# Kernel optimization log

Hardware: AMD Instinct MI355X
Metric: run time of the kernel (lower is better)

Reference implementation:

```python
import jax, jax.numpy as jnp
import numpy as np

D_MODEL = 1024
D_STATE = 32
EXPAND = 2
D_INNER = D_MODEL * EXPAND
B_SZ = 2
SEQ = 512


def setup_inputs() -> dict:
    key = jax.random.key(0)
    ks = jax.random.split(key, 10)
    x = jax.random.normal(ks[0], (B_SZ, SEQ, D_MODEL), dtype=jnp.float32)
    W_in = jax.random.normal(ks[1], (2 * D_INNER, D_MODEL), dtype=jnp.float32) * 0.02
    A_log = jax.random.uniform(ks[2], (D_INNER, D_STATE), minval=-4.0, maxval=-1.0, dtype=jnp.float32)
    W_B = jax.random.normal(ks[3], (D_STATE, D_MODEL), dtype=jnp.float32) * 0.02
    W_C = jax.random.normal(ks[4], (D_STATE, D_MODEL), dtype=jnp.float32) * 0.02
    W_dt = jax.random.normal(ks[5], (D_INNER, D_MODEL), dtype=jnp.float32) * 0.02
    b_dt = jnp.zeros((D_INNER,), dtype=jnp.float32)
    dt_bias = jnp.zeros((D_INNER,), dtype=jnp.float32) - 4.0
    rope_freq = jax.random.normal(ks[6], (D_STATE // 2,), dtype=jnp.float32) * 0.01
    ln_w = jnp.ones((D_INNER,), dtype=jnp.float32)
    ln_b = jnp.zeros((D_INNER,), dtype=jnp.float32)
    W_out = jax.random.normal(ks[7], (D_MODEL, D_INNER), dtype=jnp.float32) * 0.02
    return {"x": x, "W_in": W_in, "A_log": A_log, "W_B": W_B, "W_C": W_C,
            "W_dt": W_dt, "b_dt": b_dt, "dt_bias": dt_bias, "rope_freq": rope_freq,
            "ln_w": ln_w, "ln_b": ln_b, "W_out": W_out}


def _forward(x, W_in, A_log, W_B, W_C, W_dt, b_dt, dt_bias, rope_freq, ln_w, ln_b, W_out):
    B, L, _ = x.shape
    half = D_STATE // 2
    offset = 0

    xz = jnp.einsum('bld,ed->ble', x, W_in)                 # [B,L,2*D_INNER]
    x_inner = xz[..., :D_INNER]                             # [B,L,DI]
    z = jax.nn.silu(xz[..., D_INNER:])                      # [B,L,DI]

    A = -jnp.exp(A_log)                                     # [DI,DS]
    Bm = jnp.einsum('bld,nd->bln', x, W_B)                  # [B,L,DS]
    Cm = jnp.einsum('bld,nd->bln', x, W_C)                  # [B,L,DS]
    dt = jax.nn.softplus(jnp.einsum('bld,ed->ble', x, W_dt) + b_dt + dt_bias)  # [B,L,DI]

    # trapezoidal discretization
    dtA = dt[..., None] * A                                 # [B,L,DI,DS]
    denom = 1.0 - dtA / 2.0
    A_bar = (1.0 + dtA / 2.0) / denom                       # [B,L,DI,DS]
    B_bar = dt[..., None] / denom                           # [B,L,DI,DS]

    # per-step rope rotation angles: angle_t = rope_freq * (t + offset)
    t_idx = jnp.arange(L, dtype=jnp.float32) + offset       # [L]
    ang = t_idx[:, None] * rope_freq                        # [L,half]
    cos_a = jnp.cos(ang)
    sin_a = jnp.sin(ang)

    def step(state, inp):
        A_t, Bb_t, B_t, x_t, C_t, c_t, s_t = inp
        # state update: [B,DI,DS]
        state = A_t * state + Bb_t * B_t[:, None, :] * x_t[:, :, None]
        real = state[..., :half]
        imag = state[..., half:]
        state = jnp.concatenate([real * c_t - imag * s_t,
                                 real * s_t + imag * c_t], axis=-1)
        y_t = jnp.einsum('bds,bs->bd', state, C_t)          # [B,DI]
        return state, y_t

    state0 = jnp.zeros((B, D_INNER, D_STATE), dtype=x.dtype)
    xs = (jnp.swapaxes(A_bar, 0, 1), jnp.swapaxes(B_bar, 0, 1),
          jnp.swapaxes(Bm, 0, 1), jnp.swapaxes(x_inner, 0, 1),
          jnp.swapaxes(Cm, 0, 1), cos_a, sin_a)
    final_state, ys = jax.lax.scan(step, state0, xs)        # ys: [L,B,DI]
    out = jnp.swapaxes(ys, 0, 1) * z                        # [B,L,DI]

    # LayerNorm over last dim (eps=1e-5, torch default)
    mu = jnp.mean(out, axis=-1, keepdims=True)
    var = jnp.mean((out - mu) ** 2, axis=-1, keepdims=True)
    out = (out - mu) * jax.lax.rsqrt(var + 1e-5) * ln_w + ln_b

    out = jnp.einsum('ble,de->bld', out, W_out)             # [B,L,D_MODEL]
    return out, final_state


def reference(x, W_in, A_log, W_B, W_C, W_dt, b_dt, dt_bias, rope_freq, ln_w, ln_b, W_out):
    return _forward(x, W_in, A_log, W_B, W_C, W_dt, b_dt, dt_bias, rope_freq, ln_w, ln_b, W_out)
```

## Files before the change

### kernel.cpp

```cpp
#include <hip/hip_runtime.h>
#include <math.h>

#define B_SZ 2
#define SEQ 512
#define DM 1024
#define DI 2048
#define DS 32
#define TOK (B_SZ*SEQ)
#define NCH 8
#define CLEN (SEQ/NCH)
#define NPAIRH 32768

#define NFUSED 6272

typedef float v2f __attribute__((ext_vector_type(2)));

__device__ __forceinline__ unsigned short f2bf(float f) {
  unsigned int u = __builtin_bit_cast(unsigned int, f);
  unsigned int r = u + 0x7fffu + ((u >> 16) & 1u);
  return (unsigned short)(r >> 16);
}

static __device__ __forceinline__ v2f pk_fma(v2f a, v2f b, v2f c) {
  v2f d;
  asm("v_pk_fma_f32 %0, %1, %2, %3" : "=v"(d) : "v"(a), "v"(b), "v"(c));
  return d;
}
static __device__ __forceinline__ v2f pk_fms(v2f a, v2f b, v2f c) {
  v2f d;
  asm("v_pk_fma_f32 %0, %1, %2, %3 neg_lo:[0,0,1] neg_hi:[0,0,1]"
      : "=v"(d) : "v"(a), "v"(b), "v"(c));
  return d;
}
static __device__ __forceinline__ v2f pk_mul(v2f a, v2f b) {
  v2f d;
  asm("v_pk_mul_f32 %0, %1, %2" : "=v"(d) : "v"(a), "v"(b));
  return d;
}
static __device__ __forceinline__ v2f pk_add(v2f a, v2f b) {
  v2f d;
  asm("v_pk_add_f32 %0, %1, %2" : "=v"(d) : "v"(a), "v"(b));
  return d;
}
static __device__ __forceinline__ v2f pk_fma_b(v2f a, v2f b, v2f c) {
  v2f d;
  asm("v_pk_fma_f32 %0, %1, %2, %3 op_sel_hi:[1,0,1]"
      : "=v"(d) : "v"(a), "v"(b), "v"(c));
  return d;
}
static __device__ __forceinline__ v2f pk_mul_b(v2f a, v2f b) {
  v2f d;
  asm("v_pk_mul_f32 %0, %1, %2 op_sel_hi:[1,0]"
      : "=v"(d) : "v"(a), "v"(b));
  return d;
}

template<int CTRL>
__device__ __forceinline__ float row_ror_add(float x) {
  int s = __builtin_amdgcn_update_dpp(0, __builtin_bit_cast(int, x), CTRL, 0xf, 0xf, false);
  return x + __builtin_bit_cast(float, s);
}
__device__ __forceinline__ float row16_sum(float v) {
  v = row_ror_add<0x121>(v);
  v = row_ror_add<0x122>(v);
  v = row_ror_add<0x124>(v);
  v = row_ror_add<0x128>(v);
  return v;
}

__global__ __launch_bounds__(256) void fused_cast(const float* __restrict__ x,
                                                  const float* __restrict__ W_in,
                                                  const float* __restrict__ W_dt,
                                                  const float* __restrict__ W_B,
                                                  const float* __restrict__ W_C,
                                                  const float* __restrict__ W_out,
                                                  unsigned short* __restrict__ xb,
                                                  unsigned short* __restrict__ wcat,
                                                  unsigned short* __restrict__ wob) {
  int g = blockIdx.x * 256 + threadIdx.x;
  const float* s; unsigned short* dd; int off;
  if      (g <  131072) { s = x;     dd = xb;             off = 0; }
  else if (g <  655360) { s = W_in;  dd = wcat;           off = 131072; }
  else if (g <  917504) { s = W_dt;  dd = wcat + 4194304; off = 655360; }
  else if (g <  921600) { s = W_B;   dd = wcat + 6291456; off = 917504; }
  else if (g <  925696) { s = W_C;   dd = wcat + 6324224; off = 921600; }
  else if (g < 1187840) { s = W_out; dd = wob;            off = 925696; }
  else return;
  int i = g - off;
  float4 a = ((const float4*)s)[i * 2];
  float4 b = ((const float4*)s)[i * 2 + 1];
  union { unsigned short us[8]; uint4 v; } o;
  o.us[0] = f2bf(a.x); o.us[1] = f2bf(a.y); o.us[2] = f2bf(a.z); o.us[3] = f2bf(a.w);
  o.us[4] = f2bf(b.x); o.us[5] = f2bf(b.y); o.us[6] = f2bf(b.z); o.us[7] = f2bf(b.w);
  ((uint4*)dd)[i] = o.v;
}

typedef __attribute__((ext_vector_type(8))) short  frag8;
typedef __attribute__((ext_vector_type(4))) float  facc4;

__device__ __forceinline__ void gload_lds16(const unsigned short* g, unsigned short* l) {
  __builtin_amdgcn_global_load_lds((const __attribute__((address_space(1))) unsigned int*)g,
                                   (__attribute__((address_space(3))) unsigned int*)l, 16, 0, 0);
}
__device__ __forceinline__ void gload_lds16f(const float* g, float* l) {
  __builtin_amdgcn_global_load_lds((const __attribute__((address_space(1))) unsigned int*)g,
                                   (__attribute__((address_space(3))) unsigned int*)l, 16, 0, 0);
}

__device__ __forceinline__ float softplus_fast(float v) {
  return fmaxf(v, 0.f) + __logf(1.f + __expf(-fabsf(v)));
}

__global__ __launch_bounds__(256) void gemm1_big(const unsigned short* __restrict__ A,
                                                 const unsigned short* __restrict__ Bw,
                                                 float* __restrict__ o_xs,
                                                 float* __restrict__ o_zb,
                                                 float* __restrict__ o_dts,
                                                 float* __restrict__ o_bcb,
                                                 const float* __restrict__ b_dt,
                                                 const float* __restrict__ dt_bias) {
  __shared__ __align__(16) unsigned short As[128 * 64];
  __shared__ __align__(16) unsigned short Bs[64 * 64];
  const int K = DM;
  const int tid = threadIdx.x;
  const int w = tid >> 6, lane = tid & 63;
  const int wm = w >> 1, wn = w & 1;
  const int bid = blockIdx.x;
  const int Wk = (bid & 7) * 98 + (bid >> 3);
  const int m0 = (Wk & 7) * 128;
  const int n0 = (Wk >> 3) * 64;
  const int r = lane & 15, q = lane >> 4;
  const int srow = lane >> 3;
  const int scol = ((lane & 7) ^ srow) * 8;
  facc4 acc[4][2] = {};
  const unsigned short* Ag = A + (size_t)m0 * K;
  const unsigned short* Bg = Bw + (size_t)n0 * K;

  for (int k0 = 0; k0 < DM; k0 += 64) {
#pragma unroll
    for (int k = 0; k < 4; ++k) {
      int ch = w * 4 + k;
      gload_lds16(Ag + (size_t)(ch * 8 + srow) * K + k0 + scol, &As[ch * 512]);
    }
#pragma unroll
    for (int k = 0; k < 2; ++k) {
      int ch = w * 2 + k;
      gload_lds16(Bg + (size_t)(ch * 8 + srow) * K + k0 + scol, &Bs[ch * 512]);
    }
    __syncthreads();
#pragma unroll
    for (int kk = 0; kk < 2; ++kk) {
      frag8 af[4], bfr[2];
      const int sw = ((kk * 4 + q) ^ (r & 7)) * 8;
#pragma unroll
      for (int i = 0; i < 4; ++i)
        af[i] = *(const frag8*)&As[(wm * 64 + i * 16 + r) * 64 + sw];
#pragma unroll
      for (int jj = 0; jj < 2; ++jj)
        bfr[jj] = *(const frag8*)&Bs[(wn * 32 + jj * 16 + r) * 64 + sw];
#pragma unroll
      for (int i = 0; i < 4; ++i)
#pragma unroll
        for (int jj = 0; jj < 2; ++jj)
          acc[i][jj] = __builtin_amdgcn_mfma_f32_16x16x32_bf16(af[i], bfr[jj], acc[i][jj], 0, 0, 0);
    }
    __syncthreads();
  }

#pragma unroll
  for (int i = 0; i < 4; ++i) {
#pragma unroll
    for (int jj = 0; jj < 2; ++jj) {
      int n = n0 + wn * 32 + jj * 16 + r;
      int mb = m0 + wm * 64 + i * 16 + q * 4;
      if (n < 2048) {
#pragma unroll
        for (int rg = 0; rg < 4; ++rg)
          o_xs[(size_t)(mb + rg) * DI + n] = acc[i][jj][rg];
      } else if (n < 4096) {
#pragma unroll
        for (int rg = 0; rg < 4; ++rg)
          o_zb[(size_t)(mb + rg) * DI + (n - 2048)] = acc[i][jj][rg];
      } else if (n < 6144) {
        int d = n - 4096;
        float bias = b_dt[d] + dt_bias[d];
#pragma unroll
        for (int rg = 0; rg < 4; ++rg)
          o_dts[(size_t)(mb + rg) * DI + d] = softplus_fast(acc[i][jj][rg] + bias);
      } else if (n < 6176) {
#pragma unroll
        for (int rg = 0; rg < 4; ++rg)
          o_bcb[(size_t)(mb + rg) * DS + (n - 6144)] = acc[i][jj][rg];
      } else if (n < 6208) {
#pragma unroll
        for (int rg = 0; rg < 4; ++rg)
          o_bcb[(size_t)TOK * DS + (size_t)(mb + rg) * DS + (n - 6176)] = acc[i][jj][rg];
      }
    }
  }
}

template<int MT, int NT, int KSP>
__global__ __launch_bounds__(256) void gemm_mfma(const unsigned short* __restrict__ A,
                                                 const unsigned short* __restrict__ Bw,
                                                 int K,
                                                 float* __restrict__ o_c, int ldc) {
  __shared__ __align__(16) unsigned short As[64 * 64];
  __shared__ __align__(16) unsigned short Bs[64 * 64];
  const int tid = threadIdx.x;
  const int w = tid >> 6, lane = tid & 63;
  const int wm = w >> 1, wn = w & 1;
  const int bid = blockIdx.x;
  const int Wk = (bid & 7) * ((int)gridDim.x >> 3) + (bid >> 3);
  const int ks = Wk / (MT * NT);
  const int rem = Wk % (MT * NT);
  const int m0 = (rem % MT) * 64;
  const int n0 = (rem / MT) * 64;
  const int kLen = K / KSP, kBeg = ks * kLen;
  const int r = lane & 15, q = lane >> 4;
  const int srow = lane >> 3;
  const int scol = ((lane & 7) ^ (srow & 7)) * 8;
  facc4 acc[2][2] = {};
  const unsigned short* Ag = A + (size_t)m0 * K + kBeg;
  const unsigned short* Bg = Bw + (size_t)n0 * K + kBeg;

  for (int k0 = 0; k0 < kLen; k0 += 64) {
#pragma unroll
    for (int k = 0; k < 2; ++k) {
      int ch = w * 2 + k;
      gload_lds16(Ag + (size_t)(ch * 8 + srow) * K + k0 + scol, &As[ch * 512]);
      gload_lds16(Bg + (size_t)(ch * 8 + srow) * K + k0 + scol, &Bs[ch * 512]);
    }
    __syncthreads();
#pragma unroll
    for (int kk = 0; kk < 2; ++kk) {
      frag8 af[2], bf[2];
      const int sw = ((kk * 4 + q) ^ (r & 7)) * 8;
#pragma unroll
      for (int i = 0; i < 2; ++i)
        af[i] = *(const frag8*)&As[(wm * 32 + i * 16 + r) * 64 + sw];
#pragma unroll
      for (int jj = 0; jj < 2; ++jj)
        bf[jj] = *(const frag8*)&Bs[(wn * 32 + jj * 16 + r) * 64 + sw];
#pragma unroll
      for (int i = 0; i < 2; ++i)
#pragma unroll
        for (int jj = 0; jj < 2; ++jj)
          acc[i][jj] = __builtin_amdgcn_mfma_f32_16x16x32_bf16(af[i], bf[jj], acc[i][jj], 0, 0, 0);
    }
    __syncthreads();
  }

#pragma unroll
  for (int i = 0; i < 2; ++i) {
#pragma unroll
    for (int jj = 0; jj < 2; ++jj) {
      int n = n0 + wn * 32 + jj * 16 + r;
      int mb = m0 + wm * 32 + i * 16 + q * 4;
      float* oc = o_c + (size_t)ks * (MT * 64) * ldc;
#pragma unroll
      for (int rg = 0; rg < 4; ++rg)
        oc[(size_t)(mb + rg) * ldc + n] = acc[i][jj][rg];
    }
  }
}

__global__ __launch_bounds__(256) void addk(const float* __restrict__ p0,
                                            const float* __restrict__ p1,
                                            float* __restrict__ o) {
  int i = blockIdx.x * 256 + threadIdx.x;
  float4 a = ((const float4*)p0)[i];
  float4 b = ((const float4*)p1)[i];
  ((float4*)o)[i] = make_float4(a.x + b.x, a.y + b.y, a.z + b.z, a.w + b.w);
}

__global__ __launch_bounds__(256) void scan_p1(const float* __restrict__ xs,
                                               const float* __restrict__ dts,
                                               const float* __restrict__ bcb,
                                               const float* __restrict__ A_log,
                                               const float* __restrict__ rope,
                                               float* __restrict__ Pbuf) {
  __shared__ __align__(16) float lds[6144];
  const int blk = blockIdx.x;
  const int c = blk >> 7;
  const int sub = blk & 127;
  const int b = sub >> 6;
  const int dbase = (sub & 63) << 5;
  const int tid = threadIdx.x;
  const int wv = tid >> 6, lane = tid & 63;
  const int j = tid & 15;
  const int ca = (tid >> 4) & 15;
  const int l0 = c * CLEN;
  const size_t base = (size_t)(b * SEQ + l0);

  {
    int row = wv * 16 + (lane >> 3);
    int col = (lane & 7) << 2;
#pragma unroll
    for (int k = 0; k < 2; ++k) {
      gload_lds16f(xs  + (base + row + k * 8) * DI + dbase + col, &lds[(wv * 16 + k * 8) * 32]);
      gload_lds16f(dts + (base + row + k * 8) * DI + dbase + col, &lds[2048 + (wv * 16 + k * 8) * 32]);
    }
#pragma unroll
    for (int k = 0; k < 2; ++k) {
      int seg = wv * 2 + k;
      gload_lds16f(bcb + base * DS + seg * 256 + lane * 4, &lds[4096 + seg * 256]);
    }
  }

  const int dA = dbase + 2 * ca;
  v2f Ar, Ai;
  Ar.x = -0.5f * __expf(A_log[dA * DS + j]);
  Ar.y = -0.5f * __expf(A_log[(dA + 1) * DS + j]);
  Ai.x = -0.5f * __expf(A_log[dA * DS + j + 16]);
  Ai.y = -0.5f * __expf(A_log[(dA + 1) * DS + j + 16]);
  const float fr = rope[j];
  float sn0, cs0, sFs, cFs;
  __sincosf((float)l0 * fr, &sn0, &cs0);
  __sincosf(fr, &sFs, &cFs);
  const v2f one = {1.f, 1.f};
  const v2f two = {2.f, 2.f};
  v2f cs2 = {cs0, cs0}, sn2 = {sn0, sn0};
  const v2f cF2 = {cFs, cFs}, sF2 = {sFs, sFs};
  __syncthreads();

  v2f p00 = one, p01 = {0.f, 0.f}, p10 = {0.f, 0.f}, p11 = one;
  v2f ur = {0.f, 0.f}, ui = {0.f, 0.f};

#pragma unroll 4
  for (int tt = 0; tt < CLEN; ++tt) {
    const int ro = tt * 32;
    v2f xin = *(const v2f*)&lds[ro + 2 * ca];
    v2f dtd = *(const v2f*)&lds[2048 + ro + 2 * ca];
    v2f Br2, Bi2;
    Br2.x = lds[4096 + ro + j];
    Bi2.x = lds[4096 + ro + j + 16];
    v2f hr = pk_mul(dtd, Ar), hi = pk_mul(dtd, Ai);
    v2f invr = pk_fma(hr, pk_fma(hr, pk_add(hr, one), one), one);
    v2f invi = pk_fma(hi, pk_fma(hi, pk_add(hi, one), one), one);
    v2f dx = pk_mul(dtd, xin);
    v2f gr = pk_fma_b(dx, Br2, pk_add(ur, ur));
    v2f gi = pk_fma_b(dx, Bi2, pk_add(ui, ui));
    v2f tr = pk_fms(invr, gr, ur);
    v2f ti = pk_fms(invi, gi, ui);
    ur = pk_fms(tr, cs2, pk_mul(ti, sn2));
    ui = pk_fma(tr, sn2, pk_mul(ti, cs2));
    v2f Abr = pk_fms(invr, two, one);
    v2f Abi = pk_fms(invi, two, one);
    v2f q00 = pk_mul(Abr, p00), q01 = pk_mul(Abr, p01);
    v2f q10 = pk_mul(Abi, p10), q11 = pk_mul(Abi, p11);
    p00 = pk_fms(q00, cs2, pk_mul(q10, sn2));
    p10 = pk_fma(q00, sn2, pk_mul(q10, cs2));
    p01 = pk_fms(q01, cs2, pk_mul(q11, sn2));
    p11 = pk_fma(q01, sn2, pk_mul(q11, cs2));
    v2f ocs = cs2;
    cs2 = pk_fms(cs2, cF2, pk_mul(sn2, sF2));
    sn2 = pk_fma(sn2, cF2, pk_mul(ocs, sF2));
  }
  const int pc = (b * 1024 + (dbase >> 1) + ca) * 16 + j;
  float2* Pb2 = (float2*)Pbuf;
  Pb2[(c * 6 + 0) * NPAIRH + pc] = make_float2(p00.x, p00.y);
  Pb2[(c * 6 + 1) * NPAIRH + pc] = make_float2(p01.x, p01.y);
  Pb2[(c * 6 + 2) * NPAIRH + pc] = make_float2(p10.x, p10.y);
  Pb2[(c * 6 + 3) * NPAIRH + pc] = make_float2(p11.x, p11.y);
  Pb2[(c * 6 + 4) * NPAIRH + pc] = make_float2(ur.x, ur.y);
  Pb2[(c * 6 + 5) * NPAIRH + pc] = make_float2(ui.x, ui.y);
}

__global__ __launch_bounds__(256) void scan_p3(const float* __restrict__ xs,
                                               const float* __restrict__ dts,
                                               const float* __restrict__ bcb,
                                               const float* __restrict__ A_log,
                                               const float* __restrict__ rope,
                                               const float* __restrict__ Pbuf,
                                               float* __restrict__ y,
                                               float* __restrict__ fstate) {
  __shared__ __align__(16) float lds[8192];
  const int blk = blockIdx.x;
  const int c = blk >> 7;
  const int sub = blk & 127;
  const int b = sub >> 6;
  const int dbase = (sub & 63) << 5;
  const int tid = threadIdx.x;
  const int wv = tid >> 6, lane = tid & 63;
  const int j = tid & 15;
  const int ca = (tid >> 4) & 15;
  const int l0 = c * CLEN;
  const size_t base = (size_t)(b * SEQ + l0);

  {
    int row = wv * 16 + (lane >> 3);
    int col = (lane & 7) << 2;
#pragma unroll
    for (int k = 0; k < 2; ++k) {
      gload_lds16f(xs  + (base + row + k * 8) * DI + dbase + col, &lds[(wv * 16 + k * 8) * 32]);
      gload_lds16f(dts + (base + row + k * 8) * DI + dbase + col, &lds[2048 + (wv * 16 + k * 8) * 32]);
    }
#pragma unroll
    for (int k = 0; k < 2; ++k) {
      int seg = wv * 2 + k;
      gload_lds16f(bcb + base * DS + seg * 256 + lane * 4, &lds[4096 + seg * 256]);
      gload_lds16f(bcb + (size_t)TOK * DS + base * DS + seg * 256 + lane * 4, &lds[6144 + seg * 256]);
    }
  }

  const int dA = dbase + 2 * ca;
  v2f Ar, Ai;
  Ar.x = -0.5f * __expf(A_log[dA * DS + j]);
  Ar.y = -0.5f * __expf(A_log[(dA + 1) * DS + j]);
  Ai.x = -0.5f * __expf(A_log[dA * DS + j + 16]);
  Ai.y = -0.5f * __expf(A_log[(dA + 1) * DS + j + 16]);
  const float fr = rope[j];
  float sn0, cs0, sFs, cFs;
  __sincosf((float)l0 * fr, &sn0, &cs0);
  __sincosf(fr, &sFs, &cFs);
  const v2f one = {1.f, 1.f};
  v2f cs2 = {cs0, cs0}, sn2 = {sn0, sn0};
  const v2f cF2 = {cFs, cFs}, sF2 = {sFs, sFs};

  const int pc = (b * 1024 + (dbase >> 1) + ca) * 16 + j;
  const float2* Pb2 = (const float2*)Pbuf;
  v2f sr = {0.f, 0.f}, si = {0.f, 0.f};
  for (int k = 0; k < c; ++k) {
    float2 f;
    f = Pb2[(k * 6 + 0) * NPAIRH + pc]; v2f p00 = {f.x, f.y};
    f = Pb2[(k * 6 + 1) * NPAIRH + pc]; v2f p01 = {f.x, f.y};
    f = Pb2[(k * 6 + 2) * NPAIRH + pc]; v2f p10 = {f.x, f.y};
    f = Pb2[(k * 6 + 3) * NPAIRH + pc]; v2f p11 = {f.x, f.y};
    f = Pb2[(k * 6 + 4) * NPAIRH + pc]; v2f ur  = {f.x, f.y};
    f = Pb2[(k * 6 + 5) * NPAIRH + pc]; v2f ui  = {f.x, f.y};
    v2f nr = p00 * sr + p01 * si + ur;
    v2f ni = p10 * sr + p11 * si + ui;
    sr = nr; si = ni;
  }
  __syncthreads();

  float* yp = y + base * DI + dA;

#pragma unroll 4
  for (int tt = 0; tt < CLEN; ++tt) {
    const int ro = tt * 32;
    v2f xin = *(const v2f*)&lds[ro + 2 * ca];
    v2f dtd = *(const v2f*)&lds[2048 + ro + 2 * ca];
    v2f Br2, Bi2, Cr2, Ci2;
    Br2.x = lds[4096 + ro + j];
    Bi2.x = lds[4096 + ro + j + 16];
    Cr2.x = lds[6144 + ro + j];
    Ci2.x = lds[6144 + ro + j + 16];
    v2f hr = pk_mul(dtd, Ar), hi = pk_mul(dtd, Ai);
    v2f invr = pk_fma(hr, pk_fma(hr, pk_add(hr, one), one), one);
    v2f invi = pk_fma(hi, pk_fma(hi, pk_add(hi, one), one), one);
    v2f dx = pk_mul(dtd, xin);
    v2f gr = pk_fma_b(dx, Br2, pk_add(sr, sr));
    v2f gi = pk_fma_b(dx, Bi2, pk_add(si, si));
    v2f tr = pk_fms(invr, gr, sr);
    v2f ti = pk_fms(invi, gi, si);
    sr = pk_fms(tr, cs2, pk_mul(ti, sn2));
    si = pk_fma(tr, sn2, pk_mul(ti, cs2));
    v2f p = pk_fma_b(si, Ci2, pk_mul_b(sr, Cr2));
    float pA = row16_sum(p.x);
    float pB = row16_sum(p.y);
    if (j == 0) *(float2*)&yp[tt * DI] = make_float2(pA, pB);
    v2f ocs = cs2;
    cs2 = pk_fms(cs2, cF2, pk_mul(sn2, sF2));
    sn2 = pk_fma(sn2, cF2, pk_mul(ocs, sF2));
  }
  if (c == NCH - 1) {
    fstate[((size_t)b * DI + dA) * DS + j]          = sr.x;
    fstate[((size_t)b * DI + dA) * DS + j + 16]     = si.x;
    fstate[((size_t)b * DI + dA + 1) * DS + j]      = sr.y;
    fstate[((size_t)b * DI + dA + 1) * DS + j + 16] = si.y;
  }
}

__global__ __launch_bounds__(256) void gate_ln(const float* __restrict__ y,
                                               const float* __restrict__ zb,
                                               const float* __restrict__ lw,
                                               const float* __restrict__ lb,
                                               unsigned short* __restrict__ o) {
  int tok = blockIdx.x;
  int t = threadIdx.x;
  float g[8];
  float sum = 0.f, sq = 0.f;
#pragma unroll
  for (int i = 0; i < 8; ++i) {
    int dd = t + i * 256;
    float yv = y[(size_t)tok * DI + dd];
    float zv = zb[(size_t)tok * DI + dd];
    float sg = zv / (1.f + __expf(-zv));
    float v = yv * sg;
    g[i] = v; sum += v; sq += v * v;
  }
#pragma unroll
  for (int off = 32; off; off >>= 1) { sum += __shfl_xor(sum, off); sq += __shfl_xor(sq, off); }
  __shared__ float rs[4], rq[4];
  int w = t >> 6;
  if ((t & 63) == 0) { rs[w] = sum; rq[w] = sq; }
  __syncthreads();
  sum = rs[0] + rs[1] + rs[2] + rs[3];
  sq  = rq[0] + rq[1] + rq[2] + rq[3];
  float mu = sum * (1.f / DI);
  float var = sq * (1.f / DI) - mu * mu;
  float rstd = rsqrtf(var + 1e-5f);
#pragma unroll
  for (int i = 0; i < 8; ++i) {
    int dd = t + i * 256;
    o[(size_t)tok * DI + dd] = f2bf((g[i] - mu) * rstd * lw[dd] + lb[dd]);
  }
}

extern "C" void kernel_launch(void* const* d_in, const int* in_sizes, int n_in,
                              void* d_out, int out_size, void* d_ws, size_t ws_size,
                              hipStream_t stream) {
  const float* x       = (const float*)d_in[0];
  const float* W_in    = (const float*)d_in[1];
  const float* A_log   = (const float*)d_in[2];
  const float* W_B     = (const float*)d_in[3];
  const float* W_C     = (const float*)d_in[4];
  const float* W_dt    = (const float*)d_in[5];
  const float* b_dt    = (const float*)d_in[6];
  const float* dt_bias = (const float*)d_in[7];
  const float* rope    = (const float*)d_in[8];
  const float* ln_w    = (const float*)d_in[9];
  const float* ln_b    = (const float*)d_in[10];
  const float* W_out   = (const float*)d_in[11];
  float* out = (float*)d_out;
  float* ws = (float*)d_ws;

  float* xs   = ws;
  float* zb   = ws + 2097152;
  float* dts  = ws + 4194304;
  float* bcb  = ws + 6291456;
  unsigned short* wob  = (unsigned short*)(ws + 6356992);
  unsigned short* xb   = (unsigned short*)(ws + 7405568);
  unsigned short* wcat = (unsigned short*)(ws + 7929856);
  float* Pbuf = ws + 7929856;
  float* yb   = ws + 11141120;
  unsigned short* lnb = (unsigned short*)(ws + 13238272);
  float* Pk   = ws;
  float* fstate = out + (size_t)TOK * DM;

  fused_cast<<<4640, 256, 0, stream>>>(x, W_in, W_dt, W_B, W_C, W_out, xb, wcat, wob);
  gemm1_big<<<784, 256, 0, stream>>>(xb, wcat, xs, zb, dts, bcb, b_dt, dt_bias);
  scan_p1<<<(NCH - 1) * 128, 256, 0, stream>>>(xs, dts, bcb, A_log, rope, Pbuf);
  scan_p3<<<NCH * 128, 256, 0, stream>>>(xs, dts, bcb, A_log, rope, Pbuf, yb, fstate);
  gate_ln<<<TOK, 256, 0, stream>>>(yb, zb, ln_w, ln_b, lnb);
  gemm_mfma<16, 16, 2><<<16 * 16 * 2, 256, 0, stream>>>(lnb, wob, DI, Pk, DM);
  addk<<<(TOK * DM) / 1024, 256, 0, stream>>>(Pk, Pk + (size_t)TOK * DM, out);
}
```

Baseline: 197.4 us.

## Interleave x and dt channels and B/C real-imag pairs for vector LDS reads

The GEMM epilogue now writes x_inner and dt into one interleaved buffer (x pair, dt pair per channel pair), and stores B/C with real and imaginary halves interleaved. The scan kernels load this with fewer, wider global-to-LDS copies and read x/dt as one 128-bit LDS load and B/C as one 64-bit load, using op_sel packed FMAs to select halves. This is meant to cut LDS read instructions in the serial scan loop. In exchange the GEMM epilogue stores become strided (stride 4 floats), which may hurt its write coalescing.

```diff
diff --git a/kernel.cpp b/kernel.cpp
--- a/kernel.cpp
+++ b/kernel.cpp
@@ -14,6 +14,7 @@
 #define NFUSED 6272
 
 typedef float v2f __attribute__((ext_vector_type(2)));
+typedef float v4f __attribute__((ext_vector_type(4)));
 
 __device__ __forceinline__ unsigned short f2bf(float f) {
   unsigned int u = __builtin_bit_cast(unsigned int, f);
@@ -45,6 +46,12 @@
 static __device__ __forceinline__ v2f pk_fma_b(v2f a, v2f b, v2f c) {
   v2f d;
   asm("v_pk_fma_f32 %0, %1, %2, %3 op_sel_hi:[1,0,1]"
+      : "=v"(d) : "v"(a), "v"(b), "v"(c));
+  return d;
+}
+static __device__ __forceinline__ v2f pk_fma_bh(v2f a, v2f b, v2f c) {
+  v2f d;
+  asm("v_pk_fma_f32 %0, %1, %2, %3 op_sel:[0,1,0] op_sel_hi:[1,1,1]"
       : "=v"(d) : "v"(a), "v"(b), "v"(c));
   return d;
 }
@@ -113,9 +120,8 @@
 
 __global__ __launch_bounds__(256) void gemm1_big(const unsigned short* __restrict__ A,
                                                  const unsigned short* __restrict__ Bw,
-                                                 float* __restrict__ o_xs,
+                                                 float* __restrict__ o_xdt,
                                                  float* __restrict__ o_zb,
-                                                 float* __restrict__ o_dts,
                                                  float* __restrict__ o_bcb,
                                                  const float* __restrict__ b_dt,
                                                  const float* __restrict__ dt_bias) {
@@ -176,7 +182,7 @@
       if (n < 2048) {
 #pragma unroll
         for (int rg = 0; rg < 4; ++rg)
-          o_xs[(size_t)(mb + rg) * DI + n] = acc[i][jj][rg];
+          o_xdt[(size_t)(mb + rg) * 4096 + (n >> 1) * 4 + (n & 1)] = acc[i][jj][rg];
       } else if (n < 4096) {
 #pragma unroll
         for (int rg = 0; rg < 4; ++rg)
@@ -186,15 +192,19 @@
         float bias = b_dt[d] + dt_bias[d];
 #pragma unroll
         for (int rg = 0; rg < 4; ++rg)
-          o_dts[(size_t)(mb + rg) * DI + d] = softplus_fast(acc[i][jj][rg] + bias);
+          o_xdt[(size_t)(mb + rg) * 4096 + (d >> 1) * 4 + 2 + (d & 1)] =
+              softplus_fast(acc[i][jj][rg] + bias);
       } else if (n < 6176) {
+        int d = n - 6144;
 #pragma unroll
         for (int rg = 0; rg < 4; ++rg)
-          o_bcb[(size_t)(mb + rg) * DS + (n - 6144)] = acc[i][jj][rg];
+          o_bcb[(size_t)(mb + rg) * DS + (d & 15) * 2 + (d >> 4)] = acc[i][jj][rg];
       } else if (n < 6208) {
+        int d = n - 6176;
 #pragma unroll
         for (int rg = 0; rg < 4; ++rg)
-          o_bcb[(size_t)TOK * DS + (size_t)(mb + rg) * DS + (n - 6176)] = acc[i][jj][rg];
+          o_bcb[(size_t)TOK * DS + (size_t)(mb + rg) * DS + (d & 15) * 2 + (d >> 4)] =
+              acc[i][jj][rg];
       }
     }
   }
@@ -274,8 +284,7 @@
   ((float4*)o)[i] = make_float4(a.x + b.x, a.y + b.y, a.z + b.z, a.w + b.w);
 }
 
-__global__ __launch_bounds__(256) void scan_p1(const float* __restrict__ xs,
-                                               const float* __restrict__ dts,
+__global__ __launch_bounds__(256) void scan_p1(const float* __restrict__ xdt,
                                                const float* __restrict__ bcb,
                                                const float* __restrict__ A_log,
                                                const float* __restrict__ rope,
@@ -294,13 +303,12 @@
   const size_t base = (size_t)(b * SEQ + l0);
 
   {
-    int row = wv * 16 + (lane >> 3);
-    int col = (lane & 7) << 2;
-#pragma unroll
-    for (int k = 0; k < 2; ++k) {
-      gload_lds16f(xs  + (base + row + k * 8) * DI + dbase + col, &lds[(wv * 16 + k * 8) * 32]);
-      gload_lds16f(dts + (base + row + k * 8) * DI + dbase + col, &lds[2048 + (wv * 16 + k * 8) * 32]);
-    }
+    int t = wv * 4 + (lane >> 4);
+    int col = (lane & 15) * 4;
+#pragma unroll
+    for (int k = 0; k < 4; ++k)
+      gload_lds16f(xdt + (base + k * 16 + t) * 4096 + dbase * 2 + col,
+                   &lds[(k * 16 + wv * 4) * 64]);
 #pragma unroll
     for (int k = 0; k < 2; ++k) {
       int seg = wv * 2 + k;
@@ -329,18 +337,16 @@
 
 #pragma unroll 4
   for (int tt = 0; tt < CLEN; ++tt) {
-    const int ro = tt * 32;
-    v2f xin = *(const v2f*)&lds[ro + 2 * ca];
-    v2f dtd = *(const v2f*)&lds[2048 + ro + 2 * ca];
-    v2f Br2, Bi2;
-    Br2.x = lds[4096 + ro + j];
-    Bi2.x = lds[4096 + ro + j + 16];
-    v2f hr = pk_mul(dtd, Ar), hi = pk_mul(dtd, Ai);
+    v4f xd = *(const v4f*)&lds[tt * 64 + ca * 4];
+    v2f Bv = *(const v2f*)&lds[4096 + tt * 32 + 2 * j];
+    v2f xin = {xd.x, xd.y};
+    v2f dtd = {xd.z, xd.w};
+    v2f hr = pk_mul(dtd, Ar), hi2 = pk_mul(dtd, Ai);
     v2f invr = pk_fma(hr, pk_fma(hr, pk_add(hr, one), one), one);
-    v2f invi = pk_fma(hi, pk_fma(hi, pk_add(hi, one), one), one);
+    v2f invi = pk_fma(hi2, pk_fma(hi2, pk_add(hi2, one), one), one);
     v2f dx = pk_mul(dtd, xin);
-    v2f gr = pk_fma_b(dx, Br2, pk_add(ur, ur));
-    v2f gi = pk_fma_b(dx, Bi2, pk_add(ui, ui));
+    v2f gr = pk_fma_b (dx, Bv, pk_add(ur, ur));
+    v2f gi = pk_fma_bh(dx, Bv, pk_add(ui, ui));
     v2f tr = pk_fms(invr, gr, ur);
     v2f ti = pk_fms(invi, gi, ui);
     ur = pk_fms(tr, cs2, pk_mul(ti, sn2));
@@ -367,8 +373,7 @@
   Pb2[(c * 6 + 5) * NPAIRH + pc] = make_float2(ui.x, ui.y);
 }
 
-__global__ __launch_bounds__(256) void scan_p3(const float* __restrict__ xs,
-                                               const float* __restrict__ dts,
+__global__ __launch_bounds__(256) void scan_p3(const float* __restrict__ xdt,
                                                const float* __restrict__ bcb,
                                                const float* __restrict__ A_log,
                                                const float* __restrict__ rope,
@@ -389,18 +394,18 @@
   const size_t base = (size_t)(b * SEQ + l0);
 
   {
-    int row = wv * 16 + (lane >> 3);
-    int col = (lane & 7) << 2;
-#pragma unroll
-    for (int k = 0; k < 2; ++k) {
-      gload_lds16f(xs  + (base + row + k * 8) * DI + dbase + col, &lds[(wv * 16 + k * 8) * 32]);
-      gload_lds16f(dts + (base + row + k * 8) * DI + dbase + col, &lds[2048 + (wv * 16 + k * 8) * 32]);
-    }
+    int t = wv * 4 + (lane >> 4);
+    int col = (lane & 15) * 4;
+#pragma unroll
+    for (int k = 0; k < 4; ++k)
+      gload_lds16f(xdt + (base + k * 16 + t) * 4096 + dbase * 2 + col,
+                   &lds[(k * 16 + wv * 4) * 64]);
 #pragma unroll
     for (int k = 0; k < 2; ++k) {
       int seg = wv * 2 + k;
       gload_lds16f(bcb + base * DS + seg * 256 + lane * 4, &lds[4096 + seg * 256]);
-      gload_lds16f(bcb + (size_t)TOK * DS + base * DS + seg * 256 + lane * 4, &lds[6144 + seg * 256]);
+      gload_lds16f(bcb + (size_t)TOK * DS + base * DS + seg * 256 + lane * 4,
+                   &lds[6144 + seg * 256]);
     }
   }
 
@@ -439,25 +444,22 @@
 
 #pragma unroll 4
   for (int tt = 0; tt < CLEN; ++tt) {
-    const int ro = tt * 32;
-    v2f xin = *(const v2f*)&lds[ro + 2 * ca];
-    v2f dtd = *(const v2f*)&lds[2048 + ro + 2 * ca];
-    v2f Br2, Bi2, Cr2, Ci2;
-    Br2.x = lds[4096 + ro + j];
-    Bi2.x = lds[4096 + ro + j + 16];
-    Cr2.x = lds[6144 + ro + j];
-    Ci2.x = lds[6144 + ro + j + 16];
-    v2f hr = pk_mul(dtd, Ar), hi = pk_mul(dtd, Ai);
+    v4f xd = *(const v4f*)&lds[tt * 64 + ca * 4];
+    v2f Bv = *(const v2f*)&lds[4096 + tt * 32 + 2 * j];
+    v2f Cv = *(const v2f*)&lds[6144 + tt * 32 + 2 * j];
+    v2f xin = {xd.x, xd.y};
+    v2f dtd = {xd.z, xd.w};
+    v2f hr = pk_mul(dtd, Ar), hi2 = pk_mul(dtd, Ai);
     v2f invr = pk_fma(hr, pk_fma(hr, pk_add(hr, one), one), one);
-    v2f invi = pk_fma(hi, pk_fma(hi, pk_add(hi, one), one), one);
+    v2f invi = pk_fma(hi2, pk_fma(hi2, pk_add(hi2, one), one), one);
     v2f dx = pk_mul(dtd, xin);
-    v2f gr = pk_fma_b(dx, Br2, pk_add(sr, sr));
-    v2f gi = pk_fma_b(dx, Bi2, pk_add(si, si));
+    v2f gr = pk_fma_b (dx, Bv, pk_add(sr, sr));
+    v2f gi = pk_fma_bh(dx, Bv, pk_add(si, si));
     v2f tr = pk_fms(invr, gr, sr);
     v2f ti = pk_fms(invi, gi, si);
     sr = pk_fms(tr, cs2, pk_mul(ti, sn2));
     si = pk_fma(tr, sn2, pk_mul(ti, cs2));
-    v2f p = pk_fma_b(si, Ci2, pk_mul_b(sr, Cr2));
+    v2f p = pk_fma_bh(si, Cv, pk_mul_b(sr, Cv));
     float pA = row16_sum(p.x);
     float pB = row16_sum(p.y);
     if (j == 0) *(float2*)&yp[tt * DI] = make_float2(pA, pB);
@@ -527,9 +529,8 @@
   float* out = (float*)d_out;
   float* ws = (float*)d_ws;
 
-  float* xs   = ws;
-  float* zb   = ws + 2097152;
-  float* dts  = ws + 4194304;
+  float* xdt  = ws;
+  float* zb   = ws + 4194304;
   float* bcb  = ws + 6291456;
   unsigned short* wob  = (unsigned short*)(ws + 6356992);
   unsigned short* xb   = (unsigned short*)(ws + 7405568);
@@ -541,9 +542,9 @@
   float* fstate = out + (size_t)TOK * DM;
 
   fused_cast<<<4640, 256, 0, stream>>>(x, W_in, W_dt, W_B, W_C, W_out, xb, wcat, wob);
-  gemm1_big<<<784, 256, 0, stream>>>(xb, wcat, xs, zb, dts, bcb, b_dt, dt_bias);
-  scan_p1<<<(NCH - 1) * 128, 256, 0, stream>>>(xs, dts, bcb, A_log, rope, Pbuf);
-  scan_p3<<<NCH * 128, 256, 0, stream>>>(xs, dts, bcb, A_log, rope, Pbuf, yb, fstate);
+  gemm1_big<<<784, 256, 0, stream>>>(xb, wcat, xdt, zb, bcb, b_dt, dt_bias);
+  scan_p1<<<(NCH - 1) * 128, 256, 0, stream>>>(xdt, bcb, A_log, rope, Pbuf);
+  scan_p3<<<NCH * 128, 256, 0, stream>>>(xdt, bcb, A_log, rope, Pbuf, yb, fstate);
   gate_ln<<<TOK, 256, 0, stream>>>(yb, zb, ln_w, ln_b, lnb);
   gemm_mfma<16, 16, 2><<<16 * 16 * 2, 256, 0, stream>>>(lnb, wob, DI, Pk, DM);
   addk<<<(TOK * DM) / 1024, 256, 0, stream>>>(Pk, Pk + (size_t)TOK * DM, out);
```

After: 205.6 us. +4.1%, slower.

## Double scan chunk count and fuse split-K output GEMM reduction in-block

Applied to the files above, without the earlier changes.

Raises the number of scan chunks from 8 to 16, halving chunk length so the scan kernels launch more blocks with smaller LDS tiles and shorter serial loops. The cost is a longer cross-chunk combine and a larger Pbuf, which now moves to its own workspace region. The output GEMM replaces the split-K launch plus a separate add kernel with one 512-thread block per tile. Two 256-thread groups each cover half of K and are summed through shared memory. This drops one kernel launch and the partial-sum round trip through global memory, but halves the GEMM grid to 256 blocks.

```diff
diff --git a/kernel.cpp b/kernel.cpp
--- a/kernel.cpp
+++ b/kernel.cpp
@@ -7,7 +7,7 @@
 #define DI 2048
 #define DS 32
 #define TOK (B_SZ*SEQ)
-#define NCH 8
+#define NCH 16
 #define CLEN (SEQ/NCH)
 #define NPAIRH 32768
 
@@ -200,36 +200,36 @@
   }
 }
 
-template<int MT, int NT, int KSP>
-__global__ __launch_bounds__(256) void gemm_mfma(const unsigned short* __restrict__ A,
-                                                 const unsigned short* __restrict__ Bw,
-                                                 int K,
-                                                 float* __restrict__ o_c, int ldc) {
-  __shared__ __align__(16) unsigned short As[64 * 64];
-  __shared__ __align__(16) unsigned short Bs[64 * 64];
+__global__ __launch_bounds__(512) void gemm2_fused(const unsigned short* __restrict__ A,
+                                                   const unsigned short* __restrict__ Bw,
+                                                   float* __restrict__ o_c) {
+  __shared__ __align__(16) unsigned short As[2][64 * 64];
+  __shared__ __align__(16) unsigned short Bs[2][64 * 64];
+  const int K = DI;
   const int tid = threadIdx.x;
-  const int w = tid >> 6, lane = tid & 63;
+  const int grp = tid >> 8;
+  const int w = (tid >> 6) & 3;
+  const int lane = tid & 63;
   const int wm = w >> 1, wn = w & 1;
   const int bid = blockIdx.x;
-  const int Wk = (bid & 7) * ((int)gridDim.x >> 3) + (bid >> 3);
-  const int ks = Wk / (MT * NT);
-  const int rem = Wk % (MT * NT);
-  const int m0 = (rem % MT) * 64;
-  const int n0 = (rem / MT) * 64;
-  const int kLen = K / KSP, kBeg = ks * kLen;
+  const int Wk = (bid & 7) * 32 + (bid >> 3);
+  const int m0 = (Wk % 16) * 64;
+  const int n0 = (Wk / 16) * 64;
   const int r = lane & 15, q = lane >> 4;
   const int srow = lane >> 3;
-  const int scol = ((lane & 7) ^ (srow & 7)) * 8;
+  const int scol = ((lane & 7) ^ srow) * 8;
   facc4 acc[2][2] = {};
-  const unsigned short* Ag = A + (size_t)m0 * K + kBeg;
-  const unsigned short* Bg = Bw + (size_t)n0 * K + kBeg;
-
-  for (int k0 = 0; k0 < kLen; k0 += 64) {
+  const unsigned short* Ag = A + (size_t)m0 * K + grp * 1024;
+  const unsigned short* Bg = Bw + (size_t)n0 * K + grp * 1024;
+  unsigned short* Asg = As[grp];
+  unsigned short* Bsg = Bs[grp];
+
+  for (int k0 = 0; k0 < 1024; k0 += 64) {
 #pragma unroll
     for (int k = 0; k < 2; ++k) {
       int ch = w * 2 + k;
-      gload_lds16(Ag + (size_t)(ch * 8 + srow) * K + k0 + scol, &As[ch * 512]);
-      gload_lds16(Bg + (size_t)(ch * 8 + srow) * K + k0 + scol, &Bs[ch * 512]);
+      gload_lds16(Ag + (size_t)(ch * 8 + srow) * K + k0 + scol, &Asg[ch * 512]);
+      gload_lds16(Bg + (size_t)(ch * 8 + srow) * K + k0 + scol, &Bsg[ch * 512]);
     }
     __syncthreads();
 #pragma unroll
@@ -238,10 +238,10 @@
       const int sw = ((kk * 4 + q) ^ (r & 7)) * 8;
 #pragma unroll
       for (int i = 0; i < 2; ++i)
-        af[i] = *(const frag8*)&As[(wm * 32 + i * 16 + r) * 64 + sw];
+        af[i] = *(const frag8*)&Asg[(wm * 32 + i * 16 + r) * 64 + sw];
 #pragma unroll
       for (int jj = 0; jj < 2; ++jj)
-        bf[jj] = *(const frag8*)&Bs[(wn * 32 + jj * 16 + r) * 64 + sw];
+        bf[jj] = *(const frag8*)&Bsg[(wn * 32 + jj * 16 + r) * 64 + sw];
 #pragma unroll
       for (int i = 0; i < 2; ++i)
 #pragma unroll
@@ -251,27 +251,33 @@
     __syncthreads();
   }
 
-#pragma unroll
-  for (int i = 0; i < 2; ++i) {
-#pragma unroll
-    for (int jj = 0; jj < 2; ++jj) {
-      int n = n0 + wn * 32 + jj * 16 + r;
-      int mb = m0 + wm * 32 + i * 16 + q * 4;
-      float* oc = o_c + (size_t)ks * (MT * 64) * ldc;
-#pragma unroll
-      for (int rg = 0; rg < 4; ++rg)
-        oc[(size_t)(mb + rg) * ldc + n] = acc[i][jj][rg];
-    }
-  }
-}
-
-__global__ __launch_bounds__(256) void addk(const float* __restrict__ p0,
-                                            const float* __restrict__ p1,
-                                            float* __restrict__ o) {
-  int i = blockIdx.x * 256 + threadIdx.x;
-  float4 a = ((const float4*)p0)[i];
-  float4 b = ((const float4*)p1)[i];
-  ((float4*)o)[i] = make_float4(a.x + b.x, a.y + b.y, a.z + b.z, a.w + b.w);
+  float* red = (float*)&As[0][0];
+  if (grp == 1) {
+#pragma unroll
+    for (int i = 0; i < 2; ++i)
+#pragma unroll
+      for (int jj = 0; jj < 2; ++jj) {
+        int coln = wn * 32 + jj * 16 + r;
+        int rowb = wm * 32 + i * 16 + q * 4;
+#pragma unroll
+        for (int rg = 0; rg < 4; ++rg)
+          red[(rowb + rg) * 64 + coln] = acc[i][jj][rg];
+      }
+  }
+  __syncthreads();
+  if (grp == 0) {
+#pragma unroll
+    for (int i = 0; i < 2; ++i)
+#pragma unroll
+      for (int jj = 0; jj < 2; ++jj) {
+        int coln = wn * 32 + jj * 16 + r;
+        int rowb = wm * 32 + i * 16 + q * 4;
+#pragma unroll
+        for (int rg = 0; rg < 4; ++rg)
+          o_c[(size_t)(m0 + rowb + rg) * DM + n0 + coln] =
+              acc[i][jj][rg] + red[(rowb + rg) * 64 + coln];
+      }
+  }
 }
 
 __global__ __launch_bounds__(256) void scan_p1(const float* __restrict__ xs,
@@ -280,7 +286,7 @@
                                                const float* __restrict__ A_log,
                                                const float* __restrict__ rope,
                                                float* __restrict__ Pbuf) {
-  __shared__ __align__(16) float lds[6144];
+  __shared__ __align__(16) float lds[3072];
   const int blk = blockIdx.x;
   const int c = blk >> 7;
   const int sub = blk & 127;
@@ -294,18 +300,11 @@
   const size_t base = (size_t)(b * SEQ + l0);
 
   {
-    int row = wv * 16 + (lane >> 3);
+    int row = wv * 8 + (lane >> 3);
     int col = (lane & 7) << 2;
-#pragma unroll
-    for (int k = 0; k < 2; ++k) {
-      gload_lds16f(xs  + (base + row + k * 8) * DI + dbase + col, &lds[(wv * 16 + k * 8) * 32]);
-      gload_lds16f(dts + (base + row + k * 8) * DI + dbase + col, &lds[2048 + (wv * 16 + k * 8) * 32]);
-    }
-#pragma unroll
-    for (int k = 0; k < 2; ++k) {
-      int seg = wv * 2 + k;
-      gload_lds16f(bcb + base * DS + seg * 256 + lane * 4, &lds[4096 + seg * 256]);
-    }
+    gload_lds16f(xs  + (base + row) * DI + dbase + col, &lds[wv * 256]);
+    gload_lds16f(dts + (base + row) * DI + dbase + col, &lds[1024 + wv * 256]);
+    gload_lds16f(bcb + base * DS + wv * 256 + lane * 4, &lds[2048 + wv * 256]);
   }
 
   const int dA = dbase + 2 * ca;
@@ -331,13 +330,13 @@
   for (int tt = 0; tt < CLEN; ++tt) {
     const int ro = tt * 32;
     v2f xin = *(const v2f*)&lds[ro + 2 * ca];
-    v2f dtd = *(const v2f*)&lds[2048 + ro + 2 * ca];
+    v2f dtd = *(const v2f*)&lds[1024 + ro + 2 * ca];
     v2f Br2, Bi2;
-    Br2.x = lds[4096 + ro + j];
-    Bi2.x = lds[4096 + ro + j + 16];
-    v2f hr = pk_mul(dtd, Ar), hi = pk_mul(dtd, Ai);
+    Br2.x = lds[2048 + ro + j];
+    Bi2.x = lds[2048 + ro + j + 16];
+    v2f hr = pk_mul(dtd, Ar), hi2 = pk_mul(dtd, Ai);
     v2f invr = pk_fma(hr, pk_fma(hr, pk_add(hr, one), one), one);
-    v2f invi = pk_fma(hi, pk_fma(hi, pk_add(hi, one), one), one);
+    v2f invi = pk_fma(hi2, pk_fma(hi2, pk_add(hi2, one), one), one);
     v2f dx = pk_mul(dtd, xin);
     v2f gr = pk_fma_b(dx, Br2, pk_add(ur, ur));
     v2f gi = pk_fma_b(dx, Bi2, pk_add(ui, ui));
@@ -375,7 +374,7 @@
                                                const float* __restrict__ Pbuf,
                                                float* __restrict__ y,
                                                float* __restrict__ fstate) {
-  __shared__ __align__(16) float lds[8192];
+  __shared__ __align__(16) float lds[4096];
   const int blk = blockIdx.x;
   const int c = blk >> 7;
   const int sub = blk & 127;
@@ -389,19 +388,13 @@
   const size_t base = (size_t)(b * SEQ + l0);
 
   {
-    int row = wv * 16 + (lane >> 3);
+    int row = wv * 8 + (lane >> 3);
     int col = (lane & 7) << 2;
-#pragma unroll
-    for (int k = 0; k < 2; ++k) {
-      gload_lds16f(xs  + (base + row + k * 8) * DI + dbase + col, &lds[(wv * 16 + k * 8) * 32]);
-      gload_lds16f(dts + (base + row + k * 8) * DI + dbase + col, &lds[2048 + (wv * 16 + k * 8) * 32]);
-    }
-#pragma unroll
-    for (int k = 0; k < 2; ++k) {
-      int seg = wv * 2 + k;
-      gload_lds16f(bcb + base * DS + seg * 256 + lane * 4, &lds[4096 + seg * 256]);
-      gload_lds16f(bcb + (size_t)TOK * DS + base * DS + seg * 256 + lane * 4, &lds[6144 + seg * 256]);
-    }
+    gload_lds16f(xs  + (base + row) * DI + dbase + col, &lds[wv * 256]);
+    gload_lds16f(dts + (base + row) * DI + dbase + col, &lds[1024 + wv * 256]);
+    gload_lds16f(bcb + base * DS + wv * 256 + lane * 4, &lds[2048 + wv * 256]);
+    gload_lds16f(bcb + (size_t)TOK * DS + base * DS + wv * 256 + lane * 4,
+                 &lds[3072 + wv * 256]);
   }
 
   const int dA = dbase + 2 * ca;
@@ -441,15 +434,15 @@
   for (int tt = 0; tt < CLEN; ++tt) {
     const int ro = tt * 32;
     v2f xin = *(const v2f*)&lds[ro + 2 * ca];
-    v2f dtd = *(const v2f*)&lds[2048 + ro + 2 * ca];
+    v2f dtd = *(const v2f*)&lds[1024 + ro + 2 * ca];
     v2f Br2, Bi2, Cr2, Ci2;
-    Br2.x = lds[4096 + ro + j];
-    Bi2.x = lds[4096 + ro + j + 16];
-    Cr2.x = lds[6144 + ro + j];
-    Ci2.x = lds[6144 + ro + j + 16];
-    v2f hr = pk_mul(dtd, Ar), hi = pk_mul(dtd, Ai);
+    Br2.x = lds[2048 + ro + j];
+    Bi2.x = lds[2048 + ro + j + 16];
+    Cr2.x = lds[3072 + ro + j];
+    Ci2.x = lds[3072 + ro + j + 16];
+    v2f hr = pk_mul(dtd, Ar), hi2 = pk_mul(dtd, Ai);
     v2f invr = pk_fma(hr, pk_fma(hr, pk_add(hr, one), one), one);
-    v2f invi = pk_fma(hi, pk_fma(hi, pk_add(hi, one), one), one);
+    v2f invi = pk_fma(hi2, pk_fma(hi2, pk_add(hi2, one), one), one);
     v2f dx = pk_mul(dtd, xin);
     v2f gr = pk_fma_b(dx, Br2, pk_add(sr, sr));
     v2f gi = pk_fma_b(dx, Bi2, pk_add(si, si));
@@ -534,10 +527,9 @@
   unsigned short* wob  = (unsigned short*)(ws + 6356992);
   unsigned short* xb   = (unsigned short*)(ws + 7405568);
   unsigned short* wcat = (unsigned short*)(ws + 7929856);
-  float* Pbuf = ws + 7929856;
   float* yb   = ws + 11141120;
   unsigned short* lnb = (unsigned short*)(ws + 13238272);
-  float* Pk   = ws;
+  float* Pbuf = ws + 14286848;
   float* fstate = out + (size_t)TOK * DM;
 
   fused_cast<<<4640, 256, 0, stream>>>(x, W_in, W_dt, W_B, W_C, W_out, xb, wcat, wob);
@@ -545,6 +537,5 @@
   scan_p1<<<(NCH - 1) * 128, 256, 0, stream>>>(xs, dts, bcb, A_log, rope, Pbuf);
   scan_p3<<<NCH * 128, 256, 0, stream>>>(xs, dts, bcb, A_log, rope, Pbuf, yb, fstate);
   gate_ln<<<TOK, 256, 0, stream>>>(yb, zb, ln_w, ln_b, lnb);
-  gemm_mfma<16, 16, 2><<<16 * 16 * 2, 256, 0, stream>>>(lnb, wob, DI, Pk, DM);
-  addk<<<(TOK * DM) / 1024, 256, 0, stream>>>(Pk, Pk + (size_t)TOK * DM, out);
-}
+  gemm2_fused<<<256, 512, 0, stream>>>(lnb, wob, out);
+}
```

New measurement: 194.5 us, median of 2. About the same (-1.5%).
